# Performance work log

Measured on AMD Instinct MI355X. Metric: run time of the kernel, lower is better.

Reference implementation:

```python
import jax, jax.numpy as jnp
import numpy as np

IMG_H, IMG_W = 512.0, 512.0
PRED_SIZES = [(64, 64), (32, 32), (16, 16), (8, 8), (4, 4), (2, 2)]
ASPECT_RATIOS = [1.0, 2.0, 0.5, 3.0]
SCALES = [0.04, 0.1, 0.26, 0.42, 0.58, 0.74]
N_CLASSES = 21
CONF_THRESH = 0.01
IOU_THRESH = 0.45
TOP_K = 100
NMS_MAX = 200
XY_VAR, WH_VAR = 0.1, 0.2
NEG = -1e30  # stand-in for -inf that is safe under autodiff


def generate_boxes():
    # Standard SSD anchors (cx, cy, w, h), normalized to [0, 1].
    all_boxes = []
    for (fh, fw), s in zip(PRED_SIZES, SCALES):
        cx = (np.arange(fw, dtype=np.float32) + 0.5) / fw
        cy = (np.arange(fh, dtype=np.float32) + 0.5) / fh
        cxg, cyg = np.meshgrid(cx, cy)  # [fh, fw]
        for ar in ASPECT_RATIOS:
            w = s * np.sqrt(ar)
            h = s / np.sqrt(ar)
            b = np.stack([cxg, cyg, np.full_like(cxg, w), np.full_like(cxg, h)], axis=-1)
            all_boxes.append(b.reshape(-1, 4))
    return np.concatenate(all_boxes, axis=0).astype(np.float32)  # [21840, 4]


def setup_inputs() -> dict:
    key = jax.random.key(0)
    n_boxes = sum(fh * fw for fh, fw in PRED_SIZES) * len(ASPECT_RATIOS)
    y_pred = jax.random.normal(key, (32, n_boxes, N_CLASSES + 4), dtype=jnp.float32)
    box_tensor = jnp.asarray(generate_boxes())
    return {"y_pred": y_pred, "box_tensor": box_tensor}


def _decode(y_pred, box_tensor):
    # y_pred: [B, N, C+4], box_tensor: [N, 4] (cx, cy, w, h)
    logits = y_pred[..., :-4]
    class_ids = jnp.argmax(logits, axis=-1).astype(jnp.float32)  # [B, N]
    confidences = jnp.max(logits, axis=-1)                       # [B, N]
    a_cx, a_cy, a_w, a_h = box_tensor[:, 0], box_tensor[:, 1], box_tensor[:, 2], box_tensor[:, 3]
    cx = y_pred[..., -4] * XY_VAR * a_w + a_cx
    cy = y_pred[..., -3] * XY_VAR * a_h + a_cy
    w = jnp.exp(y_pred[..., -2] * WH_VAR) * a_w
    h = jnp.exp(y_pred[..., -1] * WH_VAR) * a_h
    xmin = jnp.clip(cx - 0.5 * w, 0.0, 1.0)
    ymin = jnp.clip(cy - 0.5 * h, 0.0, 1.0)
    xmax = jnp.clip(cx + 0.5 * w, 0.0, 1.0)
    ymax = jnp.clip(cy + 0.5 * h, 0.0, 1.0)
    # [B, N, 6]: class_id, confidence, xmin, ymin, xmax, ymax
    return jnp.stack([class_ids, confidences, xmin, ymin, xmax, ymax], axis=-1)


def _nms_image(preds):
    # preds: [N, 6]. Greedy NMS over confident, non-background boxes, then top-k.
    N = preds.shape[0]
    valid = (preds[:, 0] != 0.0) & (preds[:, 1] > CONF_THRESH)
    scores0 = jnp.where(valid, preds[:, 1], NEG)
    boxes = preds[:, 2:6]  # xmin, ymin, xmax, ymax
    areas = (boxes[:, 2] - boxes[:, 0]) * (boxes[:, 3] - boxes[:, 1])
    idxs = jnp.arange(N)

    def step(scores, _):
        i = jnp.argmax(scores)
        best = scores[i]
        ok = best > NEG * 0.5
        b = boxes[i]
        ix1 = jnp.maximum(b[0], boxes[:, 0])
        iy1 = jnp.maximum(b[1], boxes[:, 1])
        ix2 = jnp.minimum(b[2], boxes[:, 2])
        iy2 = jnp.minimum(b[3], boxes[:, 3])
        inter = jnp.maximum(ix2 - ix1, 0.0) * jnp.maximum(iy2 - iy1, 0.0)
        union = areas[i] + areas - inter
        iou = jnp.where(union > 0.0, inter / jnp.maximum(union, 1e-12), 0.0)
        suppress = (iou > IOU_THRESH) | (idxs == i)
        new_scores = jnp.where(ok & suppress, NEG, scores)
        row = jnp.where(ok, preds[i], 0.0)         # zero-pad like the TF pad path
        s = jnp.where(ok, best, 0.0)               # pad rows get score 0
        return new_scores, (row, s)

    _, (rows, sel_scores) = jax.lax.scan(step, scores0, None, length=NMS_MAX)
    # rows: [NMS_MAX, 6] in descending score order; top_k like the TF layer.
    _, ti = jax.lax.top_k(sel_scores, TOP_K)
    return rows[ti]  # [TOP_K, 6]


def reference(y_pred, box_tensor):
    preds = _decode(y_pred, box_tensor)          # [B, N, 6]
    return jax.vmap(_nms_image)(preds)           # [B, TOP_K, 6]
```

## Files before the change

kernel.cpp:

```cpp
#include <hip/hip_runtime.h>
#include <math.h>

typedef unsigned long long ull;
typedef unsigned int uint;

#define NBOX 21840
#define NPAD 22528
#define NSEG 44
#define SEGSZ 512
#define PFXS 46
#define OUTW 47
#define NWALK (NSEG*PFXS)
#define MCAP 2048
#define BATCH 32
#define NCLS 21
#define NEGV -1e30f

__device__ __forceinline__ uint key_hi(float s) {
    uint b = __float_as_uint(s);
    uint m = (uint)((int)b >> 31) | 0x80000000u;
    return ~(b ^ m);
}
__device__ __forceinline__ float key_score(uint hi) {
    uint srt = ~hi;
    uint b = (srt & 0x80000000u) ? (srt ^ 0x80000000u) : ~srt;
    return __uint_as_float(b);
}

__device__ __forceinline__ float area_of(float4 b) {
    return __fmul_rn(__fsub_rn(b.z, b.x), __fsub_rn(b.w, b.y));
}
__device__ __forceinline__ float iou_exact(float4 a, float aarea, float4 c, float carea) {
    float ix1 = fmaxf(a.x, c.x), iy1 = fmaxf(a.y, c.y);
    float ix2 = fminf(a.z, c.z), iy2 = fminf(a.w, c.w);
    float inter = __fmul_rn(fmaxf(__fsub_rn(ix2, ix1), 0.f), fmaxf(__fsub_rn(iy2, iy1), 0.f));
    float uni = __fsub_rn(__fadd_rn(aarea, carea), inter);
    return (uni > 0.f) ? __fdiv_rn(inter, fmaxf(uni, 1e-12f)) : 0.f;
}

__global__ __launch_bounds__(256) void decode_kernel(
    const float* __restrict__ y_pred, const float* __restrict__ box_tensor,
    float4* __restrict__ BX, ull* __restrict__ KS)
{
    __shared__ float st[256 * 25];
    int img = blockIdx.y;
    int b0  = blockIdx.x << 8;
    int tid = threadIdx.x;
    int nval = NBOX - b0; if (nval > 256) nval = 256;
    if (nval > 0) {
        const float* src = y_pred + ((size_t)img * NBOX + b0) * 25;
        int nf = nval * 25;
        for (int f = tid; f < nf; f += 256) st[f] = src[f];
    }
    __syncthreads();
    int i = b0 + tid;
    size_t o = (size_t)img * NPAD + i;
    if (tid < nval) {
        const float* yl = st + tid * 25;
        float best = yl[0]; int bi = 0;
        #pragma unroll
        for (int k = 1; k < NCLS; k++) { float v = yl[k]; if (v > best) { best = v; bi = k; } }
        float4 a = ((const float4*)box_tensor)[i];
        float t0 = yl[21], t1 = yl[22], t2 = yl[23], t3 = yl[24];
        float cx = __fadd_rn(__fmul_rn(__fmul_rn(t0, 0.1f), a.z), a.x);
        float cy = __fadd_rn(__fmul_rn(__fmul_rn(t1, 0.1f), a.w), a.y);
        float w  = __fmul_rn((float)exp((double)__fmul_rn(t2, 0.2f)), a.z);
        float h  = __fmul_rn((float)exp((double)__fmul_rn(t3, 0.2f)), a.w);
        float hw = __fmul_rn(0.5f, w), hh = __fmul_rn(0.5f, h);
        float xmin = fminf(fmaxf(__fsub_rn(cx, hw), 0.f), 1.f);
        float ymin = fminf(fmaxf(__fsub_rn(cy, hh), 0.f), 1.f);
        float xmax = fminf(fmaxf(__fadd_rn(cx, hw), 0.f), 1.f);
        float ymax = fminf(fmaxf(__fadd_rn(cy, hh), 0.f), 1.f);
        bool valid = (bi != 0) && (best > 0.01f);
        BX[o] = make_float4(xmin, ymin, xmax, ymax);
        uint hi = valid ? key_hi(best) : __float_as_uint(NEGV);
        KS[o] = ((ull)hi << 32) | ((uint)(i << 8)) | (uint)bi;
    } else {
        BX[o] = make_float4(0.f, 0.f, 0.f, 0.f);
        KS[o] = ((ull)__float_as_uint(NEGV) << 32) | ((uint)(i << 8));
    }
}

__global__ __launch_bounds__(256) void sort_kernel(const ull* __restrict__ KS, ull* __restrict__ KS2)
{
    __shared__ ull sk[SEGSZ];
    int seg = blockIdx.x, img = blockIdx.y;
    const ull* base = KS + (size_t)img * NPAD + (size_t)seg * SEGSZ;
    int tid = threadIdx.x;
    sk[tid] = base[tid]; sk[tid + 256] = base[tid + 256];
    __syncthreads();
    for (int k = 2; k <= SEGSZ; k <<= 1) {
        for (int j = k >> 1; j > 0; j >>= 1) {
            int i = ((tid & ~(j - 1)) << 1) | (tid & (j - 1));
            int l = i | j;
            ull a = sk[i], b = sk[l];
            if ((a > b) == ((i & k) == 0)) { sk[i] = b; sk[l] = a; }
            __syncthreads();
        }
    }
    if (tid < OUTW) KS2[(size_t)img * (NSEG * OUTW) + seg * OUTW + tid] = sk[tid];
}

__global__ __launch_bounds__(512) void nms_kernel(
    const ull* __restrict__ KS2, const ull* __restrict__ KS,
    const float4* __restrict__ BX, float* __restrict__ out)
{
    __shared__ ull klist[MCAP];
    __shared__ ull pref[NSEG];
    __shared__ float4 bbox[64];
    __shared__ float4 accbox[100];
    __shared__ float  accarea[100];

    int img = blockIdx.x, tid = threadIdx.x;
    const ull* ks2i = KS2 + (size_t)img * (NSEG * OUTW);

    for (int e = tid; e < MCAP; e += 512) {
        ull v = ~0ull;
        if (e < NWALK) { int seg = e / PFXS, q = e - seg * PFXS; v = ks2i[seg * OUTW + q]; }
        klist[e] = v;
    }
    if (tid < NSEG) pref[tid] = ks2i[tid * OUTW + PFXS];
    __syncthreads();

    for (int k = 2; k <= MCAP; k <<= 1) {
        for (int j = k >> 1; j > 0; j >>= 1) {
            for (int t = tid; t < MCAP / 2; t += 512) {
                int i = ((t & ~(j - 1)) << 1) | (t & (j - 1));
                int l = i | j;
                ull a = klist[i], b = klist[l];
                if ((a > b) == ((i & k) == 0)) { klist[i] = b; klist[l] = a; }
            }
            __syncthreads();
        }
    }

    if (tid >= 64) return;
    int lane = tid;
    const float4* BXg = BX + (size_t)img * NPAD;
    const ull*    ksg = KS + (size_t)img * NPAD;
    float* orow = out + (size_t)img * 600;

    ull cutk = ~0ull;
    for (int s = 0; s < NSEG; s++) { ull v = pref[s]; if (v < cutk) cutk = v; }

    int A = 0, stop = 0, done = 0;

    ull pk = klist[lane];
    float4 pbox = make_float4(0.f, 0.f, 0.f, 0.f);
    if (!(pk >> 63)) pbox = BXg[((uint)pk) >> 8];

    for (int base = 0; base < MCAP && !stop; base += 64) {
        ull kk = pk; float4 bb = pbox;
        {
            int c = base + 64 + lane;
            pk = (c < MCAP) ? klist[c] : ~0ull;
            if (!(pk >> 63)) pbox = BXg[((uint)pk) >> 8];
        }
        uint hi = (uint)(kk >> 32);
        uint lo = (uint)kk;
        bool valid = !(kk >> 63) && (kk < cutk);
        ull vmask = __ballot(valid);

        bbox[lane] = bb;
        float mya = area_of(bb);

        bool p = false;
        for (int a = 0; a < A; a++) {
            float4 ab = accbox[a];
            if (iou_exact(ab, accarea[a], bb, mya) > 0.45f) p = true;
        }
        ull sup = 0;
        for (int j = 0; j < 64; j++) {
            float4 bj = bbox[j];
            float aj = area_of(bj);
            if (iou_exact(bj, aj, bb, mya) > 0.45f) sup |= (1ull << j);
        }
        sup &= vmask & ((lane == 0) ? 0ull : ((~0ull) >> (64 - lane)));

        ull cand = __ballot(valid && !p);
        while (cand && A < 100) {
            int i = __ffsll(cand) - 1;
            ull sup_by_i = __ballot((sup >> i) & 1ull);
            if (lane == i) {
                accbox[A] = bb; accarea[A] = mya;
                orow[A * 6 + 0] = (float)(lo & 0xffu);
                orow[A * 6 + 1] = key_score(hi);
                orow[A * 6 + 2] = bb.x; orow[A * 6 + 3] = bb.y;
                orow[A * 6 + 4] = bb.z; orow[A * 6 + 5] = bb.w;
            }
            A++;
            cand &= ~(1ull << i);
            cand &= ~sup_by_i;
        }
        if (A >= 100) { stop = 1; done = 1; }
        else if (vmask != ~0ull) {
            stop = 1;
            int fi = __ffsll(~vmask) - 1;
            ull fk = __shfl(kk, fi);
            done = (fk >= cutk) ? (int)(cutk >> 63) : 1;
        }
        __builtin_amdgcn_wave_barrier();
    }

    if (!done && A < 100) {
        ull nextk = cutk;
        while (A < 100) {
            ull best = ~0ull;
            for (int e = lane; e < NPAD; e += 64) {
                ull kk2 = ksg[e];
                if (kk2 >= nextk && kk2 < best) best = kk2;
            }
            #pragma unroll
            for (int off = 32; off; off >>= 1) {
                ull o = __shfl_xor(best, off);
                if (o < best) best = o;
            }
            if (best >> 63) break;
            uint bhi = (uint)(best >> 32), blo = (uint)best;
            float4 cb = BXg[blo >> 8];
            float ca = area_of(cb);
            bool sup2 = false;
            #pragma unroll
            for (int t = 0; t < 2; t++) {
                int slot = lane + 64 * t;
                if (slot < A) {
                    if (iou_exact(accbox[slot], accarea[slot], cb, ca) > 0.45f) sup2 = true;
                }
            }
            if (__ballot(sup2) == 0ull) {
                if (lane == 0) {
                    accbox[A] = cb; accarea[A] = ca;
                    orow[A * 6 + 0] = (float)(blo & 0xffu);
                    orow[A * 6 + 1] = key_score(bhi);
                    orow[A * 6 + 2] = cb.x; orow[A * 6 + 3] = cb.y;
                    orow[A * 6 + 4] = cb.z; orow[A * 6 + 5] = cb.w;
                }
                A++;
            }
            nextk = best + 1;
            __builtin_amdgcn_wave_barrier();
        }
    }

    for (int r = lane; r < (100 - A) * 6; r += 64) orow[A * 6 + r] = 0.f;
}

extern "C" void kernel_launch(void* const* d_in, const int* in_sizes, int n_in,
                              void* d_out, int out_size, void* d_ws, size_t ws_size,
                              hipStream_t stream)
{
    const float* y_pred     = (const float*)d_in[0];
    const float* box_tensor = (const float*)d_in[1];
    float* out = (float*)d_out;

    size_t stride = (size_t)BATCH * NPAD;
    ull*    KS  = (ull*)d_ws;
    float4* BX  = (float4*)(KS + stride);
    ull*    KS2 = (ull*)(BX + stride);

    decode_kernel<<<dim3(NPAD / 256, BATCH), 256, 0, stream>>>(y_pred, box_tensor, BX, KS);
    sort_kernel<<<dim3(NSEG, BATCH), 256, 0, stream>>>(KS, KS2);
    nms_kernel<<<BATCH, 512, 0, stream>>>(KS2, KS, BX, out);
}
```

Before: 172.3 us.

## Fuse decode with segment sort, use shuffle bitonic stages, lazy IoU suppression

Decode and per-segment bitonic sort now run in one 512-thread kernel, and the decoded keys stay in registers, which removes a kernel launch and a global round trip of the key array. The low bitonic strides (32 and below) in both the segment sort and the NMS merge sort use wave shuffles instead of shared memory and barriers. In the greedy NMS, the full 64x64 IoU matrix is no longer built; each accepted box's suppression row is computed on demand through shuffles. The IoU division is replaced by a double-precision multiply compared against an exact threshold constant, which is meant to keep results identical while avoiding the divide. The risk is that this comparison could disagree with the reference on rare edge cases, and the fused kernel uses more shared memory per block.

```diff
diff --git a/kernel.cpp b/kernel.cpp
--- a/kernel.cpp
+++ b/kernel.cpp
@@ -5,9 +5,9 @@
 typedef unsigned int uint;
 
 #define NBOX 21840
-#define NPAD 22528
+#define SEGSZ 512
 #define NSEG 44
-#define SEGSZ 512
+#define NPAD (NSEG*SEGSZ)
 #define PFXS 46
 #define OUTW 47
 #define NWALK (NSEG*PFXS)
@@ -15,6 +15,7 @@
 #define BATCH 32
 #define NCLS 21
 #define NEGV -1e30f
+#define MIOU (15099494.5/33554432.0)
 
 __device__ __forceinline__ uint key_hi(float s) {
     uint b = __float_as_uint(s);
@@ -30,36 +31,47 @@
 __device__ __forceinline__ float area_of(float4 b) {
     return __fmul_rn(__fsub_rn(b.z, b.x), __fsub_rn(b.w, b.y));
 }
-__device__ __forceinline__ float iou_exact(float4 a, float aarea, float4 c, float carea) {
+__device__ __forceinline__ bool sup_check(float4 a, float aarea, float4 c, float carea) {
     float ix1 = fmaxf(a.x, c.x), iy1 = fmaxf(a.y, c.y);
     float ix2 = fminf(a.z, c.z), iy2 = fminf(a.w, c.w);
     float inter = __fmul_rn(fmaxf(__fsub_rn(ix2, ix1), 0.f), fmaxf(__fsub_rn(iy2, iy1), 0.f));
     float uni = __fsub_rn(__fadd_rn(aarea, carea), inter);
-    return (uni > 0.f) ? __fdiv_rn(inter, fmaxf(uni, 1e-12f)) : 0.f;
-}
-
-__global__ __launch_bounds__(256) void decode_kernel(
+    return (uni > 0.f) && ((double)inter > MIOU * (double)fmaxf(uni, 1e-12f));
+}
+
+__device__ __forceinline__ ull cex_shfl(ull v, int j, bool asc, int lane) {
+    ull pv = __shfl_xor(v, j);
+    bool keepmin = (((lane & j) == 0) == asc);
+    bool less = (v < pv);
+    return (keepmin == less) ? v : pv;
+}
+
+__global__ __launch_bounds__(512) void decode_sort_kernel(
     const float* __restrict__ y_pred, const float* __restrict__ box_tensor,
-    float4* __restrict__ BX, ull* __restrict__ KS)
+    float4* __restrict__ BX, ull* __restrict__ KS, ull* __restrict__ KS2)
 {
-    __shared__ float st[256 * 25];
-    int img = blockIdx.y;
-    int b0  = blockIdx.x << 8;
-    int tid = threadIdx.x;
-    int nval = NBOX - b0; if (nval > 256) nval = 256;
+    __shared__ float st[SEGSZ * 25];
+    __shared__ ull sk[SEGSZ];
+    int img = blockIdx.y, seg = blockIdx.x, tid = threadIdx.x;
+    int b0 = seg * SEGSZ;
+    int nval = NBOX - b0; nval = nval < 0 ? 0 : (nval > SEGSZ ? SEGSZ : nval);
     if (nval > 0) {
         const float* src = y_pred + ((size_t)img * NBOX + b0) * 25;
-        int nf = nval * 25;
-        for (int f = tid; f < nf; f += 256) st[f] = src[f];
+        int nf = nval * 25, nf4 = nf >> 2;
+        const float4* src4 = (const float4*)src;
+        float4* st4 = (float4*)st;
+        for (int f = tid; f < nf4; f += 512) st4[f] = src4[f];
+        for (int f = (nf4 << 2) + tid; f < nf; f += 512) st[f] = src[f];
     }
     __syncthreads();
     int i = b0 + tid;
     size_t o = (size_t)img * NPAD + i;
+    ull v;
     if (tid < nval) {
         const float* yl = st + tid * 25;
         float best = yl[0]; int bi = 0;
         #pragma unroll
-        for (int k = 1; k < NCLS; k++) { float v = yl[k]; if (v > best) { best = v; bi = k; } }
+        for (int k = 1; k < NCLS; k++) { float x = yl[k]; if (x > best) { best = x; bi = k; } }
         float4 a = ((const float4*)box_tensor)[i];
         float t0 = yl[21], t1 = yl[22], t2 = yl[23], t3 = yl[24];
         float cx = __fadd_rn(__fmul_rn(__fmul_rn(t0, 0.1f), a.z), a.x);
@@ -74,31 +86,26 @@
         bool valid = (bi != 0) && (best > 0.01f);
         BX[o] = make_float4(xmin, ymin, xmax, ymax);
         uint hi = valid ? key_hi(best) : __float_as_uint(NEGV);
-        KS[o] = ((ull)hi << 32) | ((uint)(i << 8)) | (uint)bi;
+        v = ((ull)hi << 32) | ((uint)(i << 8)) | (uint)bi;
     } else {
-        BX[o] = make_float4(0.f, 0.f, 0.f, 0.f);
-        KS[o] = ((ull)__float_as_uint(NEGV) << 32) | ((uint)(i << 8));
-    }
-}
-
-__global__ __launch_bounds__(256) void sort_kernel(const ull* __restrict__ KS, ull* __restrict__ KS2)
-{
-    __shared__ ull sk[SEGSZ];
-    int seg = blockIdx.x, img = blockIdx.y;
-    const ull* base = KS + (size_t)img * NPAD + (size_t)seg * SEGSZ;
-    int tid = threadIdx.x;
-    sk[tid] = base[tid]; sk[tid + 256] = base[tid + 256];
-    __syncthreads();
+        v = ((ull)__float_as_uint(NEGV) << 32) | ((uint)(i << 8));
+    }
+    int lane = tid & 63;
     for (int k = 2; k <= SEGSZ; k <<= 1) {
-        for (int j = k >> 1; j > 0; j >>= 1) {
-            int i = ((tid & ~(j - 1)) << 1) | (tid & (j - 1));
-            int l = i | j;
-            ull a = sk[i], b = sk[l];
-            if ((a > b) == ((i & k) == 0)) { sk[i] = b; sk[l] = a; }
+        for (int j = k >> 1; j >= 64; j >>= 1) {
+            sk[tid] = v; __syncthreads();
+            ull pv = sk[tid ^ j];
+            bool keepmin = (((tid & j) == 0) == ((tid & k) == 0));
+            bool less = (v < pv);
+            v = (keepmin == less) ? v : pv;
             __syncthreads();
         }
-    }
-    if (tid < OUTW) KS2[(size_t)img * (NSEG * OUTW) + seg * OUTW + tid] = sk[tid];
+        int j0 = (k >> 1) < 32 ? (k >> 1) : 32;
+        for (int j = j0; j >= 1; j >>= 1)
+            v = cex_shfl(v, j, (tid & k) == 0, lane);
+    }
+    KS[(size_t)img * NPAD + b0 + tid] = v;
+    if (tid < OUTW) KS2[(size_t)img * (NSEG * OUTW) + seg * OUTW + tid] = v;
 }
 
 __global__ __launch_bounds__(512) void nms_kernel(
@@ -107,41 +114,59 @@
 {
     __shared__ ull klist[MCAP];
     __shared__ ull pref[NSEG];
-    __shared__ float4 bbox[64];
     __shared__ float4 accbox[100];
     __shared__ float  accarea[100];
 
     int img = blockIdx.x, tid = threadIdx.x;
+    int wid = tid >> 6, lane = tid & 63;
     const ull* ks2i = KS2 + (size_t)img * (NSEG * OUTW);
 
-    for (int e = tid; e < MCAP; e += 512) {
-        ull v = ~0ull;
-        if (e < NWALK) { int seg = e / PFXS, q = e - seg * PFXS; v = ks2i[seg * OUTW + q]; }
-        klist[e] = v;
+    ull v[4];
+    #pragma unroll
+    for (int r = 0; r < 4; r++) {
+        int e = (wid << 8) + (r << 6) + lane;
+        v[r] = (e < NWALK) ? ks2i[(e / PFXS) * OUTW + (e % PFXS)] : ~0ull;
     }
     if (tid < NSEG) pref[tid] = ks2i[tid * OUTW + PFXS];
+
+    for (int k = 2; k <= MCAP; k <<= 1) {
+        int jl = k >> 1;
+        if (jl >= 64) {
+            #pragma unroll
+            for (int r = 0; r < 4; r++) klist[(wid << 8) + (r << 6) + lane] = v[r];
+            for (int j = jl; j >= 64; j >>= 1) {
+                __syncthreads();
+                for (int t = tid; t < MCAP / 2; t += 512) {
+                    int i = ((t & ~(j - 1)) << 1) | (t & (j - 1));
+                    int l = i | j;
+                    ull a = klist[i], b = klist[l];
+                    if ((a > b) == ((i & k) == 0)) { klist[i] = b; klist[l] = a; }
+                }
+            }
+            __syncthreads();
+            #pragma unroll
+            for (int r = 0; r < 4; r++) v[r] = klist[(wid << 8) + (r << 6) + lane];
+        }
+        int j0 = jl < 32 ? jl : 32;
+        for (int j = j0; j >= 1; j >>= 1) {
+            #pragma unroll
+            for (int r = 0; r < 4; r++) {
+                int e = (wid << 8) + (r << 6) + lane;
+                v[r] = cex_shfl(v[r], j, (e & k) == 0, lane);
+            }
+        }
+    }
+    #pragma unroll
+    for (int r = 0; r < 4; r++) klist[(wid << 8) + (r << 6) + lane] = v[r];
     __syncthreads();
 
-    for (int k = 2; k <= MCAP; k <<= 1) {
-        for (int j = k >> 1; j > 0; j >>= 1) {
-            for (int t = tid; t < MCAP / 2; t += 512) {
-                int i = ((t & ~(j - 1)) << 1) | (t & (j - 1));
-                int l = i | j;
-                ull a = klist[i], b = klist[l];
-                if ((a > b) == ((i & k) == 0)) { klist[i] = b; klist[l] = a; }
-            }
-            __syncthreads();
-        }
-    }
-
     if (tid >= 64) return;
-    int lane = tid;
     const float4* BXg = BX + (size_t)img * NPAD;
     const ull*    ksg = KS + (size_t)img * NPAD;
     float* orow = out + (size_t)img * 600;
 
     ull cutk = ~0ull;
-    for (int s = 0; s < NSEG; s++) { ull v = pref[s]; if (v < cutk) cutk = v; }
+    for (int s = 0; s < NSEG; s++) { ull x = pref[s]; if (x < cutk) cutk = x; }
 
     int A = 0, stop = 0, done = 0;
 
@@ -154,35 +179,27 @@
         {
             int c = base + 64 + lane;
             pk = (c < MCAP) ? klist[c] : ~0ull;
+            pbox = make_float4(0.f, 0.f, 0.f, 0.f);
             if (!(pk >> 63)) pbox = BXg[((uint)pk) >> 8];
         }
-        uint hi = (uint)(kk >> 32);
-        uint lo = (uint)kk;
         bool valid = !(kk >> 63) && (kk < cutk);
         ull vmask = __ballot(valid);
-
-        bbox[lane] = bb;
-        float mya = area_of(bb);
+        float carea = area_of(bb);
 
         bool p = false;
-        for (int a = 0; a < A; a++) {
-            float4 ab = accbox[a];
-            if (iou_exact(ab, accarea[a], bb, mya) > 0.45f) p = true;
-        }
-        ull sup = 0;
-        for (int j = 0; j < 64; j++) {
-            float4 bj = bbox[j];
-            float aj = area_of(bj);
-            if (iou_exact(bj, aj, bb, mya) > 0.45f) sup |= (1ull << j);
-        }
-        sup &= vmask & ((lane == 0) ? 0ull : ((~0ull) >> (64 - lane)));
+        for (int a = 0; a < A; a++)
+            p = p || sup_check(accbox[a], accarea[a], bb, carea);
 
         ull cand = __ballot(valid && !p);
         while (cand && A < 100) {
-            int i = __ffsll(cand) - 1;
-            ull sup_by_i = __ballot((sup >> i) & 1ull);
+            int i = __ffsll((ull)cand) - 1;
+            float4 ib = make_float4(__shfl(bb.x, i), __shfl(bb.y, i),
+                                    __shfl(bb.z, i), __shfl(bb.w, i));
+            float ia = __shfl(carea, i);
+            ull row = __ballot(sup_check(ib, ia, bb, carea));
             if (lane == i) {
-                accbox[A] = bb; accarea[A] = mya;
+                accbox[A] = bb; accarea[A] = carea;
+                uint hi = (uint)(kk >> 32), lo = (uint)kk;
                 orow[A * 6 + 0] = (float)(lo & 0xffu);
                 orow[A * 6 + 1] = key_score(hi);
                 orow[A * 6 + 2] = bb.x; orow[A * 6 + 3] = bb.y;
@@ -190,17 +207,18 @@
             }
             A++;
             cand &= ~(1ull << i);
-            cand &= ~sup_by_i;
+            cand &= ~row;
         }
         if (A >= 100) { stop = 1; done = 1; }
         else if (vmask != ~0ull) {
             stop = 1;
-            int fi = __ffsll(~vmask) - 1;
+            int fi = __ffsll((ull)~vmask) - 1;
             ull fk = __shfl(kk, fi);
             done = (fk >= cutk) ? (int)(cutk >> 63) : 1;
         }
         __builtin_amdgcn_wave_barrier();
     }
+    if (!stop) done = (int)(cutk >> 63);
 
     if (!done && A < 100) {
         ull nextk = cutk;
@@ -212,8 +230,8 @@
             }
             #pragma unroll
             for (int off = 32; off; off >>= 1) {
-                ull o = __shfl_xor(best, off);
-                if (o < best) best = o;
+                ull oo = __shfl_xor(best, off);
+                if (oo < best) best = oo;
             }
             if (best >> 63) break;
             uint bhi = (uint)(best >> 32), blo = (uint)best;
@@ -223,9 +241,7 @@
             #pragma unroll
             for (int t = 0; t < 2; t++) {
                 int slot = lane + 64 * t;
-                if (slot < A) {
-                    if (iou_exact(accbox[slot], accarea[slot], cb, ca) > 0.45f) sup2 = true;
-                }
+                if (slot < A && sup_check(accbox[slot], accarea[slot], cb, ca)) sup2 = true;
             }
             if (__ballot(sup2) == 0ull) {
                 if (lane == 0) {
@@ -258,7 +274,6 @@
     float4* BX  = (float4*)(KS + stride);
     ull*    KS2 = (ull*)(BX + stride);
 
-    decode_kernel<<<dim3(NPAD / 256, BATCH), 256, 0, stream>>>(y_pred, box_tensor, BX, KS);
-    sort_kernel<<<dim3(NSEG, BATCH), 256, 0, stream>>>(KS, KS2);
+    decode_sort_kernel<<<dim3(NSEG, BATCH), 512, 0, stream>>>(y_pred, box_tensor, BX, KS, KS2);
     nms_kernel<<<BATCH, 512, 0, stream>>>(KS2, KS, BX, out);
 }
```

After: 154.9 us. -10.1%, faster.
